# Performance work log

Measured on AMD Instinct MI355X. Metric: run time of the kernel, lower is better.

## Reference

```python
import jax, jax.numpy as jnp
import numpy as np

N = 8_000_000
THETA_W = 1.9  # physics-loss weight in forward()
EPS_DPDT = 1e-12
# Fixed config: bulk_modulus_model='tangent' (non-const), air_dissolution_model='on', air_fraction>0


def _drho_mix_dp(p, rho_L_atm, beta_L_atm, beta_gain, air_fraction, rho_g_atm,
                 polytropic_index, p_atm, p_crit, p_min):
    # mixture_density_derivative, vectorized over p (shape [N,1])
    p_used = jnp.maximum(p, p_min)
    L = p_crit - p_atm
    x = (p_used - p_atm) / L
    theta_mid = 1.0 - 3.0 * x**2 + 2.0 * x**3           # smoothstep between p_atm and p_crit
    theta = jnp.where(p_used <= p_atm, 1.0,
                      jnp.where(p_used >= p_crit, 0.0, theta_mid))
    dtheta_mid = 6.0 * (p_used - p_atm) * (p_used - p_crit) / L**3
    dtheta_dp = jnp.where((p_used <= p_atm) | (p_used >= p_crit), 0.0, dtheta_mid)

    afr = air_fraction / (1.0 - air_fraction)
    pr = (p_atm / p_used) ** (1.0 / polytropic_index)
    p_denom = afr * pr * theta
    p_ratio = afr * pr * (theta / (p_used * polytropic_index) - dtheta_dp)

    base = 1.0 + beta_gain * (p_used - p_atm) / beta_L_atm
    exp_term = base ** (-1.0 - 1.0 / beta_gain) / beta_L_atm

    rho_mix_init = rho_L_atm + rho_g_atm * afr
    denom = beta_L_atm * exp_term * base + p_denom
    return rho_mix_init * (exp_term + p_ratio) / denom**2


def setup_inputs() -> dict:
    key = jax.random.key(0)
    k1, k2, k3, k4 = jax.random.split(key, 4)
    outputs_P = jax.random.uniform(k1, (N, 1), dtype=jnp.float32) * 50.0  # p = 0.1*outputs_P in [0,5) MPa
    targets_P = outputs_P + 0.1 * jax.random.normal(k2, (N, 1), dtype=jnp.float32)
    dpdt = 0.5 * jax.random.normal(k3, (N, 1), dtype=jnp.float32)
    mdot_A = 0.01 * jax.random.normal(k4, (N, 1), dtype=jnp.float32)
    return {
        "targets_P": targets_P,
        "dpdt": dpdt,
        "mdot_A": mdot_A,
        "V": jnp.float32(1e-3),
        "outputs_P": outputs_P,
        "rho_L_atm": jnp.float32(850.0),
        "beta_L_atm": jnp.float32(1500.0),   # MPa
        "beta_gain": jnp.float32(10.0),
        "air_fraction": jnp.float32(0.005),
        "rho_g_atm": jnp.float32(1.2),
        "polytropic_index": jnp.float32(1.4),
        "p_atm": jnp.float32(0.101325),       # MPa
        "p_crit": jnp.float32(3.0),           # MPa
        "p_min": jnp.float32(0.01),           # MPa
    }


def reference(targets_P, dpdt, mdot_A, V, outputs_P, rho_L_atm, beta_L_atm,
              beta_gain, air_fraction, rho_g_atm, polytropic_index, p_atm,
              p_crit, p_min):
    drho = _drho_mix_dp(outputs_P * 0.1, rho_L_atm, beta_L_atm, beta_gain,
                        air_fraction, rho_g_atm, polytropic_index,
                        p_atm, p_crit, p_min)                      # [N,1]
    loss_physics = jnp.abs(V * drho * dpdt - mdot_A)                # [N,1]
    loss_M = jnp.abs(outputs_P - targets_P)                         # [N,1]
    per_sample = loss_M + THETA_W * loss_physics
    mask = jnp.abs(dpdt) >= EPS_DPDT                                # skip ~zero dpdt samples
    return jnp.sum(jnp.where(mask, per_sample, 0.0))
```

## Files before the change

### kernel.cpp

```cpp
#include <hip/hip_runtime.h>

#define THREADS 256
#define ITER    4

struct Consts {
    float p_min, p_atm, p_crit;
    float invL;
    float c_dth;
    float afr;
    float inv_n;
    float bg_over_bL;
    float inv_bL;
    float rho_mix_init;
    float V;
    float log2_patm;
    float pc1, pc2, pc3, pc4;
};

__device__ __forceinline__ float pow1p(float u, const Consts& c) {
    return fmaf(u, fmaf(u, fmaf(u, fmaf(u, c.pc4, c.pc3), c.pc2), c.pc1), 1.0f);
}

__device__ __forceinline__ float loss_elem(float oP, float tP, float dp, float md,
                                           const Consts& c) {
    float p  = 0.1f * oP;
    float pu = fmaxf(p, c.p_min);
    float dpa = pu - c.p_atm;
    float x = dpa * c.invL;
    float theta_mid = fmaf(x * x, fmaf(2.0f, x, -3.0f), 1.0f);
    bool lo = (pu <= c.p_atm);
    bool hi = (pu >= c.p_crit);
    float theta  = lo ? 1.0f : (hi ? 0.0f : theta_mid);
    float dtheta = (lo || hi) ? 0.0f : c.c_dth * dpa * (pu - c.p_crit);

    float inv_pu = __builtin_amdgcn_rcpf(pu);
    float lg_pu = __builtin_amdgcn_logf(pu);
    float pr = __builtin_amdgcn_exp2f(c.inv_n * (c.log2_patm - lg_pu));
    float apr = c.afr * pr;
    float p_denom = apr * theta;
    float p_ratio = apr * fmaf(theta * c.inv_n, inv_pu, -dtheta);

    float u  = dpa * c.bg_over_bL;
    float pb = pow1p(u, c);
    float exp_term = pb * c.inv_bL;
    float denom = fmaf(pb, u, pb) + p_denom;
    float inv_denom = __builtin_amdgcn_rcpf(denom);
    float drho = c.rho_mix_init * (exp_term + p_ratio) * inv_denom * inv_denom;

    float lp = fabsf(fmaf(c.V * dp, drho, -md));
    float lm = fabsf(oP - tP);
    float res = fmaf(1.9f, lp, lm);
    return (fabsf(dp) >= 1e-12f) ? res : 0.0f;
}

__device__ __forceinline__ float quad(const float4& o, const float4& t,
                                      const float4& d, const float4& m,
                                      const Consts& c) {
    return loss_elem(o.x, t.x, d.x, m.x, c)
         + loss_elem(o.y, t.y, d.y, m.y, c)
         + loss_elem(o.z, t.z, d.z, m.z, c)
         + loss_elem(o.w, t.w, d.w, m.w, c);
}

__device__ __forceinline__ Consts make_consts(
    const float* sV, const float* s_rhoL, const float* s_betaL,
    const float* s_bgain, const float* s_airfr, const float* s_rhog,
    const float* s_poly, const float* s_patm, const float* s_pcrit,
    const float* s_pmin) {
    Consts c;
    float beta_L = *s_betaL;
    float bgain  = *s_bgain;
    float airfr  = *s_airfr;
    float poly   = *s_poly;
    float patm   = *s_patm;
    float pcrit  = *s_pcrit;
    float L = pcrit - patm;
    c.p_min = *s_pmin;
    c.p_atm = patm;
    c.p_crit = pcrit;
    c.invL = 1.0f / L;
    c.c_dth = 6.0f / (L * L * L);
    c.afr = airfr / (1.0f - airfr);
    c.inv_n = 1.0f / poly;
    c.bg_over_bL = bgain / beta_L;
    c.inv_bL = 1.0f / beta_L;
    c.rho_mix_init = fmaf(*s_rhog, c.afr, *s_rhoL);
    c.V = *sV;
    c.log2_patm = __builtin_amdgcn_logf(patm);
    float a = -1.0f - 1.0f / bgain;
    c.pc1 = a;
    c.pc2 = a * (a - 1.0f) * 0.5f;
    c.pc3 = c.pc2 * (a - 2.0f) * (1.0f / 3.0f);
    c.pc4 = c.pc3 * (a - 3.0f) * 0.25f;
    return c;
}

#define SB() __builtin_amdgcn_sched_barrier(0)

__global__ __launch_bounds__(THREADS, 4) void loss_kernel(
    const float* __restrict__ targets_P,
    const float* __restrict__ dpdt,
    const float* __restrict__ mdot_A,
    const float* __restrict__ outputs_P,
    const float* __restrict__ sV,
    const float* __restrict__ s_rhoL,
    const float* __restrict__ s_betaL,
    const float* __restrict__ s_bgain,
    const float* __restrict__ s_airfr,
    const float* __restrict__ s_rhog,
    const float* __restrict__ s_poly,
    const float* __restrict__ s_patm,
    const float* __restrict__ s_pcrit,
    const float* __restrict__ s_pmin,
    float* __restrict__ partials,
    int n, int nfull)
{
    const int n4 = n >> 2;
    const float4* o4 = (const float4*)outputs_P;
    const float4* t4 = (const float4*)targets_P;
    const float4* d4 = (const float4*)dpdt;
    const float4* m4 = (const float4*)mdot_A;

    const Consts c = make_consts(sV, s_rhoL, s_betaL, s_bgain, s_airfr,
                                 s_rhog, s_poly, s_patm, s_pcrit, s_pmin);

    float acc = 0.0f;

    if ((int)blockIdx.x < nfull) {
        const int s0 = blockIdx.x * (THREADS * ITER) + threadIdx.x;
        float4 oa, ta, da, ma, ob, tb, db, mb;

        oa = o4[s0];              ta = t4[s0];
        da = d4[s0];              ma = m4[s0];
        SB();
        ob = o4[s0 + THREADS];    tb = t4[s0 + THREADS];
        db = d4[s0 + THREADS];    mb = m4[s0 + THREADS];
        SB();
        acc += quad(oa, ta, da, ma, c);
        SB();
        oa = o4[s0 + 2*THREADS];  ta = t4[s0 + 2*THREADS];
        da = d4[s0 + 2*THREADS];  ma = m4[s0 + 2*THREADS];
        SB();
        acc += quad(ob, tb, db, mb, c);
        SB();
        ob = o4[s0 + 3*THREADS];  tb = t4[s0 + 3*THREADS];
        db = d4[s0 + 3*THREADS];  mb = m4[s0 + 3*THREADS];
        SB();
        acc += quad(oa, ta, da, ma, c);
        SB();
        acc += quad(ob, tb, db, mb, c);
    } else {
        for (int idx = nfull * (THREADS * ITER) + threadIdx.x; idx < n4;
             idx += THREADS) {
            float4 oo = o4[idx], tt = t4[idx], dd = d4[idx], mm = m4[idx];
            acc += quad(oo, tt, dd, mm, c);
        }
        for (int j = (n4 << 2) + threadIdx.x; j < n; j += THREADS) {
            acc += loss_elem(outputs_P[j], targets_P[j], dpdt[j], mdot_A[j], c);
        }
    }

    for (int off = 32; off > 0; off >>= 1)
        acc += __shfl_down(acc, off, 64);
    __shared__ float wsum[THREADS / 64];
    int lane = threadIdx.x & 63, wid = threadIdx.x >> 6;
    if (lane == 0) wsum[wid] = acc;
    __syncthreads();
    if (threadIdx.x == 0) {
        float bsum = 0.0f;
        #pragma unroll
        for (int v = 0; v < THREADS / 64; ++v) bsum += wsum[v];
        partials[blockIdx.x] = bsum;
    }
}

__global__ __launch_bounds__(256) void loss_final_kernel(
    const float* __restrict__ partials, float* __restrict__ out, int nparts)
{
    double acc = 0.0;
    for (int i = threadIdx.x; i < nparts; i += blockDim.x)
        acc += (double)partials[i];
    for (int off = 32; off > 0; off >>= 1)
        acc += __shfl_down(acc, off, 64);
    __shared__ double wsum[4];
    int lane = threadIdx.x & 63, wid = threadIdx.x >> 6;
    if (lane == 0) wsum[wid] = acc;
    __syncthreads();
    if (threadIdx.x == 0) {
        double s = 0.0;
        #pragma unroll
        for (int w = 0; w < 4; ++w) s += wsum[w];
        out[0] = (float)s;
    }
}

extern "C" void kernel_launch(void* const* d_in, const int* in_sizes, int n_in,
                              void* d_out, int out_size, void* d_ws, size_t ws_size,
                              hipStream_t stream) {
    const float* targets_P = (const float*)d_in[0];
    const float* dpdt      = (const float*)d_in[1];
    const float* mdot_A    = (const float*)d_in[2];
    const float* sV        = (const float*)d_in[3];
    const float* outputs_P = (const float*)d_in[4];
    const float* s_rhoL    = (const float*)d_in[5];
    const float* s_betaL   = (const float*)d_in[6];
    const float* s_bgain   = (const float*)d_in[7];
    const float* s_airfr   = (const float*)d_in[8];
    const float* s_rhog    = (const float*)d_in[9];
    const float* s_poly    = (const float*)d_in[10];
    const float* s_patm    = (const float*)d_in[11];
    const float* s_pcrit   = (const float*)d_in[12];
    const float* s_pmin    = (const float*)d_in[13];

    int n  = in_sizes[0];
    int n4 = n >> 2;
    int nfull = n4 / (THREADS * ITER);
    int nblocks = nfull + 1;

    float* partials = (float*)d_ws;

    loss_kernel<<<nblocks, THREADS, 0, stream>>>(
        targets_P, dpdt, mdot_A, outputs_P,
        sV, s_rhoL, s_betaL, s_bgain, s_airfr, s_rhog, s_poly,
        s_patm, s_pcrit, s_pmin,
        partials, n, nfull);

    loss_final_kernel<<<1, 256, 0, stream>>>(partials, (float*)d_out, nblocks);
}
```

Measured before the change: 167.5 us.

## Halve per-block work, issue all loads upfront, write per-wave partials

Each block now processes two float4 chunks per thread instead of four, and all eight loads are issued together before the constants are computed, with the sched barriers removed. The intra-block shared-memory reduction and __syncthreads are replaced by each wave writing its own partial, so the final kernel sums four times as many values. The aim is more memory-level parallelism from more blocks and less block-level sync. In exchange the grid roughly doubles, which adds block launch overhead, and the single-block final reduction has to read about 8x more partials than before.

```diff
diff --git a/kernel.cpp b/kernel.cpp
--- a/kernel.cpp
+++ b/kernel.cpp
@@ -1,7 +1,8 @@
 #include <hip/hip_runtime.h>
 
 #define THREADS 256
-#define ITER    4
+#define NWAVES  (THREADS / 64)
+#define CHUNKS  2
 
 struct Consts {
     float p_min, p_atm, p_crit;
@@ -95,8 +96,6 @@
     return c;
 }
 
-#define SB() __builtin_amdgcn_sched_barrier(0)
-
 __global__ __launch_bounds__(THREADS, 4) void loss_kernel(
     const float* __restrict__ targets_P,
     const float* __restrict__ dpdt,
@@ -121,36 +120,22 @@
     const float4* d4 = (const float4*)dpdt;
     const float4* m4 = (const float4*)mdot_A;
 
-    const Consts c = make_consts(sV, s_rhoL, s_betaL, s_bgain, s_airfr,
-                                 s_rhog, s_poly, s_patm, s_pcrit, s_pmin);
-
     float acc = 0.0f;
 
     if ((int)blockIdx.x < nfull) {
-        const int s0 = blockIdx.x * (THREADS * ITER) + threadIdx.x;
-        float4 oa, ta, da, ma, ob, tb, db, mb;
-
-        oa = o4[s0];              ta = t4[s0];
-        da = d4[s0];              ma = m4[s0];
-        SB();
-        ob = o4[s0 + THREADS];    tb = t4[s0 + THREADS];
-        db = d4[s0 + THREADS];    mb = m4[s0 + THREADS];
-        SB();
+        const int s0 = blockIdx.x * (THREADS * CHUNKS) + threadIdx.x;
+        const int s1 = s0 + THREADS;
+        float4 oa = o4[s0], ta = t4[s0], da = d4[s0], ma = m4[s0];
+        float4 ob = o4[s1], tb = t4[s1], db = d4[s1], mb = m4[s1];
+
+        const Consts c = make_consts(sV, s_rhoL, s_betaL, s_bgain, s_airfr,
+                                     s_rhog, s_poly, s_patm, s_pcrit, s_pmin);
         acc += quad(oa, ta, da, ma, c);
-        SB();
-        oa = o4[s0 + 2*THREADS];  ta = t4[s0 + 2*THREADS];
-        da = d4[s0 + 2*THREADS];  ma = m4[s0 + 2*THREADS];
-        SB();
-        acc += quad(ob, tb, db, mb, c);
-        SB();
-        ob = o4[s0 + 3*THREADS];  tb = t4[s0 + 3*THREADS];
-        db = d4[s0 + 3*THREADS];  mb = m4[s0 + 3*THREADS];
-        SB();
-        acc += quad(oa, ta, da, ma, c);
-        SB();
         acc += quad(ob, tb, db, mb, c);
     } else {
-        for (int idx = nfull * (THREADS * ITER) + threadIdx.x; idx < n4;
+        const Consts c = make_consts(sV, s_rhoL, s_betaL, s_bgain, s_airfr,
+                                     s_rhog, s_poly, s_patm, s_pcrit, s_pmin);
+        for (int idx = nfull * (THREADS * CHUNKS) + threadIdx.x; idx < n4;
              idx += THREADS) {
             float4 oo = o4[idx], tt = t4[idx], dd = d4[idx], mm = m4[idx];
             acc += quad(oo, tt, dd, mm, c);
@@ -162,16 +147,9 @@
 
     for (int off = 32; off > 0; off >>= 1)
         acc += __shfl_down(acc, off, 64);
-    __shared__ float wsum[THREADS / 64];
     int lane = threadIdx.x & 63, wid = threadIdx.x >> 6;
-    if (lane == 0) wsum[wid] = acc;
-    __syncthreads();
-    if (threadIdx.x == 0) {
-        float bsum = 0.0f;
-        #pragma unroll
-        for (int v = 0; v < THREADS / 64; ++v) bsum += wsum[v];
-        partials[blockIdx.x] = bsum;
-    }
+    if (lane == 0)
+        partials[blockIdx.x * NWAVES + wid] = acc;
 }
 
 __global__ __launch_bounds__(256) void loss_final_kernel(
@@ -214,8 +192,9 @@
 
     int n  = in_sizes[0];
     int n4 = n >> 2;
-    int nfull = n4 / (THREADS * ITER);
+    int nfull = n4 / (THREADS * CHUNKS);
     int nblocks = nfull + 1;
+    int nparts = nblocks * NWAVES;
 
     float* partials = (float*)d_ws;
 
@@ -225,5 +204,5 @@
         s_patm, s_pcrit, s_pmin,
         partials, n, nfull);
 
-    loss_final_kernel<<<1, 256, 0, stream>>>(partials, (float*)d_out, nblocks);
-}
+    loss_final_kernel<<<1, 256, 0, stream>>>(partials, (float*)d_out, nparts);
+}
```

After: 181.6 us. 1.08x slower.
